# Kernel tuning notes

Hardware: AMD Instinct MI355X
Metric: run time of the kernel (lower is better)

Reference implementation:

```python
import jax, jax.numpy as jnp
import numpy as np


def setup_inputs() -> dict:
    key = jax.random.key(0)
    ks = jax.random.split(key, 6)
    B, Tq, Tv, H, A = 32, 1, 4096, 1024, 512
    return {
        "query": jax.random.normal(ks[0], (B, Tq, H), dtype=jnp.float32),
        "value": jax.random.normal(ks[1], (B, Tv, H), dtype=jnp.float32),
        # weights stored [in, out] (transpose of torch Linear's [out, in])
        "W_Q": jax.random.normal(ks[2], (H, A), dtype=jnp.float32) * 0.02,
        "W_V": jax.random.normal(ks[3], (H, A), dtype=jnp.float32) * 0.02,
        "bias": jax.random.uniform(ks[4], (A,), minval=-0.1, maxval=0.1, dtype=jnp.float32),
        "fc_w": jax.random.normal(ks[5], (A, 1), dtype=jnp.float32) * 0.02,
    }


def reference(query, value, W_Q, W_V, bias, fc_w):
    # query: [B, 1, H], value: [B, Tv, H]
    q_proj = jnp.einsum("bqh,ha->bqa", query, W_Q)          # [B, 1, A]
    v_proj = jnp.einsum("bth,ha->bta", value, W_V)          # [B, Tv, A]
    energy = jnp.tanh(q_proj + v_proj + bias)               # [B, Tv, A] (broadcast over Tv)
    attn_score = jnp.einsum("bta,ao->bt", energy, fc_w)     # [B, Tv]
    align = jax.nn.softmax(attn_score, axis=-1)             # [B, Tv]
    context = jnp.einsum("bt,bth->bh", align, value)        # [B, H]
    return context
```

## Files before the change

### kernel.cpp

```cpp
#include <hip/hip_runtime.h>
#include <hip/hip_bf16.h>
#include <math.h>

#define HH 1024
#define AA 512
#define TV 4096
#define NB 32

typedef __bf16 v8bf __attribute__((ext_vector_type(8)));
typedef float v4f __attribute__((ext_vector_type(4)));

__device__ __forceinline__ float fast_tanh(float x) {
  float e = __expf(2.0f * x);
  return 1.0f - 2.0f / (e + 1.0f);
}

__device__ __forceinline__ void load_lds16(const void* g, void* l) {
  __builtin_amdgcn_global_load_lds(
      (const __attribute__((address_space(1))) void*)g,
      (__attribute__((address_space(3))) void*)l, 16, 0, 0);
}

__global__ void k_wt(const float* __restrict__ wv, __bf16* __restrict__ wt2) {
  int idx = blockIdx.x * 256 + threadIdx.x;
  int n = idx >> 7;
  int cl = idx & 127;
  int g = cl >> 2, c = cl & 3;
  int sw = (n >> 1) & 3;
  int ks = g * 32 + ((c ^ sw) & 3) * 8;
  v8bf o;
  #pragma unroll
  for (int j = 0; j < 8; ++j) o[j] = (__bf16)wv[(size_t)(ks + j) * AA + n];
  *(v8bf*)&wt2[(size_t)n * HH + g * 32 + c * 8] = o;
}

__global__ void k_qb(const float* __restrict__ query, const float* __restrict__ wq,
                     const float* __restrict__ bias, float* __restrict__ qb) {
  int b = blockIdx.x, hc = blockIdx.y;
  int a = threadIdx.x;
  __shared__ float ql[256];
  if (a < 256) ql[a] = query[b * HH + hc * 256 + a];
  __syncthreads();
  float s = (hc == 0) ? bias[a] : 0.0f;
  const float* w = wq + (size_t)(hc * 256) * AA + a;
  #pragma unroll 8
  for (int h = 0; h < 256; ++h) s += ql[h] * w[(size_t)h * AA];
  atomicAdd(&qb[b * AA + a], s);
}

#define BM 64
#define BK 32
#define LDA 40

__launch_bounds__(256, 2)
__global__ void k_score(const float* __restrict__ value, const __bf16* __restrict__ wt2,
                        const float* __restrict__ qb, const float* __restrict__ fc,
                        float* __restrict__ scores) {
  __shared__ __align__(16) __bf16 As[BM * LDA];
  __shared__ __align__(16) __bf16 Bs[AA * BK];
  __shared__ float s_red[BM * 4];

  const int tid  = threadIdx.x;
  const int lane = tid & 63, w = tid >> 6;
  const int quad = lane >> 4, l15 = lane & 15;
  const int swl  = (l15 >> 1) & 3;
  const int bcol = ((quad ^ swl) & 3) * 8;

  const size_t m0 = (size_t)blockIdx.x * BM;
  const float* Ag = value + m0 * HH;

  const int ar = tid >> 2, ac = (tid & 3) * 8;
  const int brow_l = lane >> 2, bchunk = (lane & 3) * 8;

  v4f acc[4][8];
  #pragma unroll
  for (int i = 0; i < 4; ++i)
    #pragma unroll
    for (int n = 0; n < 8; ++n) { acc[i][n][0]=0.f; acc[i][n][1]=0.f; acc[i][n][2]=0.f; acc[i][n][3]=0.f; }

  const float* ap0 = Ag + (size_t)ar * HH + ac;
  float4 a0 = *(const float4*)ap0;
  float4 a1 = *(const float4*)(ap0 + 4);

  for (int kk = 0; kk < HH; kk += BK) {
    __syncthreads();
    #pragma unroll
    for (int i = 0; i < 8; ++i) {
      int r0 = w * 128 + i * 16;
      load_lds16(wt2 + (size_t)(r0 + brow_l) * HH + kk + bchunk, (void*)&Bs[r0 * BK]);
    }
    {
      v8bf av;
      av[0]=(__bf16)a0.x; av[1]=(__bf16)a0.y; av[2]=(__bf16)a0.z; av[3]=(__bf16)a0.w;
      av[4]=(__bf16)a1.x; av[5]=(__bf16)a1.y; av[6]=(__bf16)a1.z; av[7]=(__bf16)a1.w;
      *(v8bf*)&As[ar * LDA + ac] = av;
    }
    __syncthreads();
    if (kk + BK < HH) {
      const float* apn = Ag + (size_t)ar * HH + kk + BK + ac;
      a0 = *(const float4*)apn;
      a1 = *(const float4*)(apn + 4);
    }
    v8bf af[4], bfr[8];
    #pragma unroll
    for (int mt = 0; mt < 4; ++mt)
      af[mt] = *(v8bf*)&As[(mt * 16 + l15) * LDA + quad * 8];
    #pragma unroll
    for (int nt = 0; nt < 8; ++nt) {
      int n = w * 128 + nt * 16 + l15;
      bfr[nt] = *(v8bf*)&Bs[n * BK + bcol];
    }
    #pragma unroll
    for (int mt = 0; mt < 4; ++mt)
      #pragma unroll
      for (int nt = 0; nt < 8; ++nt)
        acc[mt][nt] = __builtin_amdgcn_mfma_f32_16x16x32_bf16(af[mt], bfr[nt], acc[mt][nt], 0, 0, 0);
  }

  const int bb = blockIdx.x >> 6;
  const int t0 = (blockIdx.x & 63) * BM;
  float fcl[8], qbl[8];
  #pragma unroll
  for (int nt = 0; nt < 8; ++nt) {
    int col = w * 128 + nt * 16 + l15;
    fcl[nt] = fc[col];
    qbl[nt] = qb[bb * AA + col];
  }
  #pragma unroll
  for (int mt = 0; mt < 4; ++mt) {
    #pragma unroll
    for (int j = 0; j < 4; ++j) {
      float p = 0.0f;
      #pragma unroll
      for (int nt = 0; nt < 8; ++nt)
        p += fcl[nt] * fast_tanh(acc[mt][nt][j] + qbl[nt]);
      p += __shfl_xor(p, 1);
      p += __shfl_xor(p, 2);
      p += __shfl_xor(p, 4);
      p += __shfl_xor(p, 8);
      if (l15 == 0) s_red[(mt * 16 + quad * 4 + j) * 4 + w] = p;
    }
  }
  __syncthreads();
  if (tid < BM) {
    float s = s_red[tid * 4 + 0] + s_red[tid * 4 + 1] + s_red[tid * 4 + 2] + s_red[tid * 4 + 3];
    scores[(size_t)bb * TV + t0 + tid] = s;
  }
}

__global__ void k_softmax(float* __restrict__ scores) {
  int b = blockIdx.x;
  int tid = threadIdx.x;
  float* s = scores + (size_t)b * TV;
  float local[16];
  float mx = -1e30f;
  #pragma unroll
  for (int i = 0; i < 16; ++i) { local[i] = s[i * 256 + tid]; mx = fmaxf(mx, local[i]); }
  __shared__ float red[8];
  #pragma unroll
  for (int o = 32; o > 0; o >>= 1) mx = fmaxf(mx, __shfl_xor(mx, o));
  int wv = tid >> 6;
  if ((tid & 63) == 0) red[wv] = mx;
  __syncthreads();
  mx = fmaxf(fmaxf(red[0], red[1]), fmaxf(red[2], red[3]));
  float sum = 0.0f;
  #pragma unroll
  for (int i = 0; i < 16; ++i) { local[i] = __expf(local[i] - mx); sum += local[i]; }
  #pragma unroll
  for (int o = 32; o > 0; o >>= 1) sum += __shfl_xor(sum, o);
  if ((tid & 63) == 0) red[4 + wv] = sum;
  __syncthreads();
  float inv = 1.0f / (red[4] + red[5] + red[6] + red[7]);
  #pragma unroll
  for (int i = 0; i < 16; ++i) s[i * 256 + tid] = local[i] * inv;
}

__global__ void k_ctx_partial(const float* __restrict__ value, const float* __restrict__ align,
                              float* __restrict__ partial, int TC, int NC) {
  int tc = blockIdx.x, b = blockIdx.y;
  int tid = threadIdx.x;
  extern __shared__ float al[];
  for (int i = tid; i < TC; i += 256) al[i] = align[(size_t)b * TV + (size_t)tc * TC + i];
  __syncthreads();
  const float* vp = value + ((size_t)b * TV + (size_t)tc * TC) * HH + tid * 4;
  float ax = 0.f, ay = 0.f, az = 0.f, aw = 0.f;
  #pragma unroll 8
  for (int t = 0; t < TC; ++t) {
    float4 v = *(const float4*)(vp + (size_t)t * HH);
    float a = al[t];
    ax = fmaf(a, v.x, ax); ay = fmaf(a, v.y, ay);
    az = fmaf(a, v.z, az); aw = fmaf(a, v.w, aw);
  }
  float4 o; o.x = ax; o.y = ay; o.z = az; o.w = aw;
  *(float4*)&partial[((size_t)(b * NC + tc)) * HH + tid * 4] = o;
}

__global__ void k_ctx_reduce(const float* __restrict__ partial, float* __restrict__ out, int NC) {
  int g = blockIdx.x * 256 + threadIdx.x;
  int b = g >> 10, h = g & 1023;
  float s = 0.0f;
  for (int c = 0; c < NC; ++c) s += partial[((size_t)(b * NC + c)) * HH + h];
  out[g] = s;
}

extern "C" void kernel_launch(void* const* d_in, const int* in_sizes, int n_in,
                              void* d_out, int out_size, void* d_ws, size_t ws_size,
                              hipStream_t stream) {
  const float* query = (const float*)d_in[0];
  const float* value = (const float*)d_in[1];
  const float* wq    = (const float*)d_in[2];
  const float* wv    = (const float*)d_in[3];
  const float* bias  = (const float*)d_in[4];
  const float* fc    = (const float*)d_in[5];
  float* out = (float*)d_out;

  char* ws = (char*)d_ws;
  __bf16* wt2   = (__bf16*)ws;
  float*  qb    = (float*)(ws + (1 << 20));
  float*  scores= (float*)(ws + (1 << 20) + (1 << 16));
  size_t  base  = (1 << 20) + (1 << 16) + (1 << 19);
  float*  partial = (float*)(ws + base);

  int NC = 64;
  while (NC > 1 && base + (size_t)NB * NC * HH * 4 > ws_size) NC >>= 1;
  int TC = TV / NC;

  hipMemsetAsync(qb, 0, NB * AA * sizeof(float), stream);
  k_wt<<<256, 256, 0, stream>>>(wv, wt2);
  k_qb<<<dim3(NB, 4), 512, 0, stream>>>(query, wq, bias, qb);
  k_score<<<(NB * TV) / BM, 256, 0, stream>>>(value, wt2, qb, fc, scores);
  k_softmax<<<NB, 256, 0, stream>>>(scores);
  k_ctx_partial<<<dim3(NC, NB), 256, TC * sizeof(float), stream>>>(value, scores, partial, TC, NC);
  k_ctx_reduce<<<(NB * HH) / 256, 256, 0, stream>>>(partial, out, NC);
}
```

Before: 941.8 us.

## Double-buffer score GEMM with 128-row tiles and 8-wave blocks

The score GEMM kernel now uses 128-row tiles with 512 threads arranged as a 2x4 wave grid, so each block of W_V^T tiles in LDS is reused across twice as many value rows. LDS buffers for A and B are double-buffered, with the next tiles prefetched ahead using manual waitcnt and raw barriers, and MFMA issue runs at raised priority. The aim is to halve W_V reload traffic and hide global-load latency behind MFMA work. In exchange, LDS use roughly doubles and the hand-placed vmcnt counts must match the exact order of issued loads, which may limit occupancy or break correctness if the compiler reorders memory operations.

```diff
diff --git a/kernel.cpp b/kernel.cpp
--- a/kernel.cpp
+++ b/kernel.cpp
@@ -48,20 +48,21 @@
   atomicAdd(&qb[b * AA + a], s);
 }
 
-#define BM 64
+#define BM 128
 #define BK 32
 #define LDA 40
 
-__launch_bounds__(256, 2)
+__launch_bounds__(512, 2)
 __global__ void k_score(const float* __restrict__ value, const __bf16* __restrict__ wt2,
                         const float* __restrict__ qb, const float* __restrict__ fc,
                         float* __restrict__ scores) {
-  __shared__ __align__(16) __bf16 As[BM * LDA];
-  __shared__ __align__(16) __bf16 Bs[AA * BK];
+  __shared__ __align__(16) __bf16 As[2][BM * LDA];
+  __shared__ __align__(16) __bf16 Bs[2][AA * BK];
   __shared__ float s_red[BM * 4];
 
   const int tid  = threadIdx.x;
   const int lane = tid & 63, w = tid >> 6;
+  const int wr = w >> 2, wc = w & 3;
   const int quad = lane >> 4, l15 = lane & 15;
   const int swl  = (l15 >> 1) & 3;
   const int bcol = ((quad ^ swl) & 3) * 8;
@@ -79,50 +80,111 @@
     for (int n = 0; n < 8; ++n) { acc[i][n][0]=0.f; acc[i][n][1]=0.f; acc[i][n][2]=0.f; acc[i][n][3]=0.f; }
 
   const float* ap0 = Ag + (size_t)ar * HH + ac;
-  float4 a0 = *(const float4*)ap0;
-  float4 a1 = *(const float4*)(ap0 + 4);
-
-  for (int kk = 0; kk < HH; kk += BK) {
-    __syncthreads();
-    #pragma unroll
-    for (int i = 0; i < 8; ++i) {
-      int r0 = w * 128 + i * 16;
-      load_lds16(wt2 + (size_t)(r0 + brow_l) * HH + kk + bchunk, (void*)&Bs[r0 * BK]);
+
+  #pragma unroll
+  for (int i = 0; i < 4; ++i) {
+    int r0 = w * 64 + i * 16;
+    load_lds16(wt2 + (size_t)(r0 + brow_l) * HH + bchunk, (void*)&Bs[0][r0 * BK]);
+  }
+  float4 x0 = *(const float4*)ap0;
+  float4 x1 = *(const float4*)(ap0 + 4);
+  float4 y0 = *(const float4*)(ap0 + BK);
+  float4 y1 = *(const float4*)(ap0 + BK + 4);
+  asm volatile("s_waitcnt vmcnt(2)" ::: "memory");
+  {
+    v8bf av;
+    av[0]=(__bf16)x0.x; av[1]=(__bf16)x0.y; av[2]=(__bf16)x0.z; av[3]=(__bf16)x0.w;
+    av[4]=(__bf16)x1.x; av[5]=(__bf16)x1.y; av[6]=(__bf16)x1.z; av[7]=(__bf16)x1.w;
+    *(v8bf*)&As[0][ar * LDA + ac] = av;
+  }
+  asm volatile("s_waitcnt lgkmcnt(0)" ::: "memory");
+  __builtin_amdgcn_s_barrier();
+
+  for (int tt = 0; tt < HH / BK; tt += 2) {
+    {
+      const int t = tt;
+      const int kb = (t + 1 < HH / BK) ? (t + 1) * BK : 0;
+      #pragma unroll
+      for (int i = 0; i < 4; ++i) {
+        int r0 = w * 64 + i * 16;
+        load_lds16(wt2 + (size_t)(r0 + brow_l) * HH + kb + bchunk, (void*)&Bs[1][r0 * BK]);
+      }
+      const int ka = (t + 2 < HH / BK) ? (t + 2) * BK : 0;
+      x0 = *(const float4*)(ap0 + ka);
+      x1 = *(const float4*)(ap0 + ka + 4);
+      asm volatile("s_waitcnt vmcnt(6)" ::: "memory");
+      {
+        v8bf av;
+        av[0]=(__bf16)y0.x; av[1]=(__bf16)y0.y; av[2]=(__bf16)y0.z; av[3]=(__bf16)y0.w;
+        av[4]=(__bf16)y1.x; av[5]=(__bf16)y1.y; av[6]=(__bf16)y1.z; av[7]=(__bf16)y1.w;
+        *(v8bf*)&As[1][ar * LDA + ac] = av;
+      }
+      v8bf af[4], bfr[8];
+      #pragma unroll
+      for (int mt = 0; mt < 4; ++mt)
+        af[mt] = *(v8bf*)&As[0][(wr * 64 + mt * 16 + l15) * LDA + quad * 8];
+      #pragma unroll
+      for (int nt = 0; nt < 8; ++nt) {
+        int n = wc * 128 + nt * 16 + l15;
+        bfr[nt] = *(v8bf*)&Bs[0][n * BK + bcol];
+      }
+      __builtin_amdgcn_s_setprio(1);
+      #pragma unroll
+      for (int mt = 0; mt < 4; ++mt)
+        #pragma unroll
+        for (int nt = 0; nt < 8; ++nt)
+          acc[mt][nt] = __builtin_amdgcn_mfma_f32_16x16x32_bf16(af[mt], bfr[nt], acc[mt][nt], 0, 0, 0);
+      __builtin_amdgcn_s_setprio(0);
+      asm volatile("s_waitcnt vmcnt(2)" ::: "memory");
+      asm volatile("s_waitcnt lgkmcnt(0)" ::: "memory");
+      __builtin_amdgcn_s_barrier();
     }
     {
-      v8bf av;
-      av[0]=(__bf16)a0.x; av[1]=(__bf16)a0.y; av[2]=(__bf16)a0.z; av[3]=(__bf16)a0.w;
-      av[4]=(__bf16)a1.x; av[5]=(__bf16)a1.y; av[6]=(__bf16)a1.z; av[7]=(__bf16)a1.w;
-      *(v8bf*)&As[ar * LDA + ac] = av;
+      const int t = tt + 1;
+      const int kb = (t + 1 < HH / BK) ? (t + 1) * BK : 0;
+      #pragma unroll
+      for (int i = 0; i < 4; ++i) {
+        int r0 = w * 64 + i * 16;
+        load_lds16(wt2 + (size_t)(r0 + brow_l) * HH + kb + bchunk, (void*)&Bs[0][r0 * BK]);
+      }
+      const int ka = (t + 2 < HH / BK) ? (t + 2) * BK : 0;
+      y0 = *(const float4*)(ap0 + ka);
+      y1 = *(const float4*)(ap0 + ka + 4);
+      asm volatile("s_waitcnt vmcnt(6)" ::: "memory");
+      {
+        v8bf av;
+        av[0]=(__bf16)x0.x; av[1]=(__bf16)x0.y; av[2]=(__bf16)x0.z; av[3]=(__bf16)x0.w;
+        av[4]=(__bf16)x1.x; av[5]=(__bf16)x1.y; av[6]=(__bf16)x1.z; av[7]=(__bf16)x1.w;
+        *(v8bf*)&As[0][ar * LDA + ac] = av;
+      }
+      v8bf af[4], bfr[8];
+      #pragma unroll
+      for (int mt = 0; mt < 4; ++mt)
+        af[mt] = *(v8bf*)&As[1][(wr * 64 + mt * 16 + l15) * LDA + quad * 8];
+      #pragma unroll
+      for (int nt = 0; nt < 8; ++nt) {
+        int n = wc * 128 + nt * 16 + l15;
+        bfr[nt] = *(v8bf*)&Bs[1][n * BK + bcol];
+      }
+      __builtin_amdgcn_s_setprio(1);
+      #pragma unroll
+      for (int mt = 0; mt < 4; ++mt)
+        #pragma unroll
+        for (int nt = 0; nt < 8; ++nt)
+          acc[mt][nt] = __builtin_amdgcn_mfma_f32_16x16x32_bf16(af[mt], bfr[nt], acc[mt][nt], 0, 0, 0);
+      __builtin_amdgcn_s_setprio(0);
+      asm volatile("s_waitcnt vmcnt(2)" ::: "memory");
+      asm volatile("s_waitcnt lgkmcnt(0)" ::: "memory");
+      __builtin_amdgcn_s_barrier();
     }
-    __syncthreads();
-    if (kk + BK < HH) {
-      const float* apn = Ag + (size_t)ar * HH + kk + BK + ac;
-      a0 = *(const float4*)apn;
-      a1 = *(const float4*)(apn + 4);
-    }
-    v8bf af[4], bfr[8];
-    #pragma unroll
-    for (int mt = 0; mt < 4; ++mt)
-      af[mt] = *(v8bf*)&As[(mt * 16 + l15) * LDA + quad * 8];
-    #pragma unroll
-    for (int nt = 0; nt < 8; ++nt) {
-      int n = w * 128 + nt * 16 + l15;
-      bfr[nt] = *(v8bf*)&Bs[n * BK + bcol];
-    }
-    #pragma unroll
-    for (int mt = 0; mt < 4; ++mt)
-      #pragma unroll
-      for (int nt = 0; nt < 8; ++nt)
-        acc[mt][nt] = __builtin_amdgcn_mfma_f32_16x16x32_bf16(af[mt], bfr[nt], acc[mt][nt], 0, 0, 0);
-  }
-
-  const int bb = blockIdx.x >> 6;
-  const int t0 = (blockIdx.x & 63) * BM;
+  }
+
+  const int bb = blockIdx.x >> 5;
+  const int t0 = (blockIdx.x & 31) * BM;
   float fcl[8], qbl[8];
   #pragma unroll
   for (int nt = 0; nt < 8; ++nt) {
-    int col = w * 128 + nt * 16 + l15;
+    int col = wc * 128 + nt * 16 + l15;
     fcl[nt] = fc[col];
     qbl[nt] = qb[bb * AA + col];
   }
@@ -138,7 +200,7 @@
       p += __shfl_xor(p, 2);
       p += __shfl_xor(p, 4);
       p += __shfl_xor(p, 8);
-      if (l15 == 0) s_red[(mt * 16 + quad * 4 + j) * 4 + w] = p;
+      if (l15 == 0) s_red[(wr * 64 + mt * 16 + quad * 4 + j) * 4 + wc] = p;
     }
   }
   __syncthreads();
@@ -228,7 +290,7 @@
   hipMemsetAsync(qb, 0, NB * AA * sizeof(float), stream);
   k_wt<<<256, 256, 0, stream>>>(wv, wt2);
   k_qb<<<dim3(NB, 4), 512, 0, stream>>>(query, wq, bias, qb);
-  k_score<<<(NB * TV) / BM, 256, 0, stream>>>(value, wt2, qb, fc, scores);
+  k_score<<<(NB * TV) / BM, 512, 0, stream>>>(value, wt2, qb, fc, scores);
   k_softmax<<<NB, 256, 0, stream>>>(scores);
   k_ctx_partial<<<dim3(NC, NB), 256, TC * sizeof(float), stream>>>(value, scores, partial, TC, NC);
   k_ctx_reduce<<<(NB * HH) / 256, 256, 0, stream>>>(partial, out, NC);
```

After: 1.010 ms. 7.3% more time.
